# Kernel optimization log

Hardware: AMD Instinct MI355X
Metric: run time of the kernel (lower is better)

The kernel has to match this reference:

```python
import jax, jax.numpy as jnp
import numpy as np

B, T, D, H = 2, 2048, 1024, 16
DH = D // H

def setup_inputs() -> dict:
    key = jax.random.key(0)
    ks = jax.random.split(key, 6)
    s = 0.02
    return {
        "x": jax.random.normal(ks[0], (B, T, D), jnp.float32),
        "Wq": jax.random.normal(ks[1], (D, D), jnp.float32) * s,
        "Wk": jax.random.normal(ks[2], (D, D), jnp.float32) * s,
        "Wv": jax.random.normal(ks[3], (D, D), jnp.float32) * s,
        "Wo": jax.random.normal(ks[4], (D, D), jnp.float32) * s,
        "bo": jnp.zeros((D,), jnp.float32),
    }

def reference(x, Wq, Wk, Wv, Wo, bo):
    Bx, Tx, _ = x.shape
    # project and split heads: [B, H, T, DH]
    q = (x @ Wq).reshape(Bx, Tx, H, DH).transpose(0, 2, 1, 3)
    k = (x @ Wk).reshape(Bx, Tx, H, DH).transpose(0, 2, 1, 3)
    v = (x @ Wv).reshape(Bx, Tx, H, DH).transpose(0, 2, 1, 3)
    scores = jnp.einsum("bhqd,bhkd->bhqk", q, k)  # [B,H,T,T]
    causal = jnp.triu(jnp.ones((Tx, Tx), bool), k=1)  # True above diagonal
    scores = jnp.where(causal, -jnp.inf, scores)
    # original scales AFTER masking (equivalent math)
    w = jax.nn.softmax(scores / jnp.sqrt(jnp.float32(DH)), axis=-1)
    # dropout p=0.0 -> identity
    ctx = jnp.einsum("bhqk,bhkd->bhqd", w, v)
    ctx = ctx.transpose(0, 2, 1, 3).reshape(Bx, Tx, D)
    return ctx @ Wo + bo
```

## Files before the change

kernel.cpp:

```cpp
#include <hip/hip_runtime.h>
#include <hip/hip_bf16.h>


typedef __bf16 bf16x8 __attribute__((ext_vector_type(8)));
typedef __bf16 bf16x4 __attribute__((ext_vector_type(4)));
typedef float  f32x4  __attribute__((ext_vector_type(4)));

#define Bx 2
#define Tx 2048
#define Dx 1024
#define Hx 16
#define DHx 64

__device__ __constant__ unsigned char JTAB[47][3] = {
    {16, 0, 17},
    {31, 0, 16}, {31, 16, 16}, {30, 0, 16}, {15, 0, 16},
    {30, 16, 15}, {29, 0, 15}, {29, 15, 15}, {28, 0, 15}, {14, 0, 15},
    {28, 15, 14}, {27, 0, 14}, {27, 14, 14}, {26, 0, 14}, {13, 0, 14},
    {26, 14, 13}, {25, 0, 13}, {25, 13, 13}, {24, 0, 13}, {12, 0, 13},
    {24, 13, 12}, {23, 0, 12}, {23, 12, 12}, {22, 0, 12}, {11, 0, 12},
    {22, 12, 11}, {21, 0, 11}, {21, 11, 11}, {20, 0, 11}, {10, 0, 11},
    {20, 11, 10}, {19, 0, 10}, {19, 10, 10}, {18, 0, 10}, {9, 0, 10},
    {18, 10, 9}, {17, 0, 9}, {17, 9, 9}, {8, 0, 9},
    {7, 0, 8}, {6, 0, 7}, {5, 0, 6}, {4, 0, 5}, {3, 0, 4}, {2, 0, 3},
    {1, 0, 2}, {0, 0, 1}
};

__global__ __launch_bounds__(256) void prep(const float* __restrict__ x,
                                            const float* __restrict__ W0,
                                            const float* __restrict__ W1,
                                            const float* __restrict__ W2,
                                            const float* __restrict__ W3,
                                            __bf16* __restrict__ xb,
                                            __bf16* __restrict__ Wt) {
    const int z = blockIdx.z;
    if (z == 0) {
        const int blk = blockIdx.y * 16 + blockIdx.x;
        const float* xp = x + (size_t)blk * 16384;
        __bf16* xo = xb + (size_t)blk * 16384;
#pragma unroll
        for (int i = 0; i < 16; i++) {
            float4 v = *(const float4*)(xp + i * 1024 + threadIdx.x * 4);
            bf16x4 o;
            o[0] = (__bf16)v.x; o[1] = (__bf16)v.y; o[2] = (__bf16)v.z; o[3] = (__bf16)v.w;
            *(bf16x4*)(xo + i * 1024 + threadIdx.x * 4) = o;
        }
        return;
    }
    __shared__ float tile[64][65];
    const float* W = (z == 1) ? W0 : (z == 2) ? W1 : (z == 3) ? W2 : W3;
    __bf16* o = Wt + (size_t)(z - 1) * Dx * Dx;
    int k0 = blockIdx.x * 64, n0 = blockIdx.y * 64;
    int t = threadIdx.x;
    int cc = t & 63, rbase = t >> 6;
#pragma unroll
    for (int i = 0; i < 16; i++) {
        int rr = rbase + i * 4;
        tile[rr][cc] = W[(size_t)(k0 + rr) * Dx + n0 + cc];
    }
    __syncthreads();
#pragma unroll
    for (int i = 0; i < 16; i++) {
        int rr = rbase + i * 4;
        o[(size_t)(n0 + rr) * Dx + k0 + cc] = (__bf16)tile[cc][rr];
    }
}

static __device__ __forceinline__ void gload16(const __bf16* g, __bf16* l) {
    __builtin_amdgcn_global_load_lds((const __attribute__((address_space(1))) void*)g,
                                     (__attribute__((address_space(3))) void*)l, 16, 0, 0);
}

__global__ __launch_bounds__(256, 3) void gemm_qkv(const __bf16* __restrict__ A,
                                                   const __bf16* __restrict__ BT,
                                                   __bf16* __restrict__ Qb,
                                                   __bf16* __restrict__ Kb,
                                                   __bf16* __restrict__ Vt) {
    __shared__ __bf16 As[2][128 * 32];
    __shared__ __bf16 Bs[2][128 * 32];
    const int t = threadIdx.x;
    const int lane = t & 63, wave = t >> 6;
    const int lane15 = lane & 15, quad = lane >> 4;
    const int m0 = blockIdx.x * 128, n0 = blockIdx.y * 128;
    const int wm = wave & 1, wn = wave >> 1;

    const int sr = wave * 16 + (lane >> 2);
    const int sc = (lane & 3) * 8;
    const __bf16* Ag = A + (size_t)(m0 + sr) * Dx + sc;
    const __bf16* Bg = BT + (size_t)(n0 + sr) * Dx + sc;
    __bf16* As00 = &As[0][(wave * 16) * 32];
    __bf16* As01 = &As[0][(64 + wave * 16) * 32];
    __bf16* As10 = &As[1][(wave * 16) * 32];
    __bf16* As11 = &As[1][(64 + wave * 16) * 32];
    __bf16* Bs00 = &Bs[0][(wave * 16) * 32];
    __bf16* Bs01 = &Bs[0][(64 + wave * 16) * 32];
    __bf16* Bs10 = &Bs[1][(wave * 16) * 32];
    __bf16* Bs11 = &Bs[1][(64 + wave * 16) * 32];

    f32x4 acc[4][4];
#pragma unroll
    for (int i = 0; i < 4; i++)
#pragma unroll
        for (int j = 0; j < 4; j++) acc[i][j] = (f32x4){0.f, 0.f, 0.f, 0.f};

    for (int k0 = 0; k0 < Dx; k0 += 64) {
        gload16(Ag, As00);
        gload16(Ag + 64 * Dx, As01);
        gload16(Ag + 32, As10);
        gload16(Ag + 64 * Dx + 32, As11);
        gload16(Bg, Bs00);
        gload16(Bg + 64 * Dx, Bs01);
        gload16(Bg + 32, Bs10);
        gload16(Bg + 64 * Dx + 32, Bs11);
        Ag += 64; Bg += 64;
        __syncthreads();
#pragma unroll
        for (int half = 0; half < 2; half++) {
            bf16x8 af[4], bfr[4];
#pragma unroll
            for (int i = 0; i < 4; i++)
                af[i] = *(const bf16x8*)&As[half][(wm * 64 + i * 16 + lane15) * 32 + quad * 8];
#pragma unroll
            for (int j = 0; j < 4; j++)
                bfr[j] = *(const bf16x8*)&Bs[half][(wn * 64 + j * 16 + lane15) * 32 + quad * 8];
#pragma unroll
            for (int mt = 0; mt < 4; mt++)
#pragma unroll
                for (int nt = 0; nt < 4; nt++)
                    acc[mt][nt] = __builtin_amdgcn_mfma_f32_16x16x32_bf16(af[mt], bfr[nt], acc[mt][nt], 0, 0, 0);
        }
        __syncthreads();
    }

    const int z = n0 >> 10;
    if (z < 2) {
        __bf16* outp = z ? Kb : Qb;
        const float scale = z ? 1.0f : 0.18033688011112042f;
#pragma unroll
        for (int mt = 0; mt < 4; mt++)
#pragma unroll
            for (int nt = 0; nt < 4; nt++) {
                const int cc = (n0 + wn * 64 + nt * 16 + lane15) & 1023;
                const int h = cc >> 6, dh = cc & 63;
#pragma unroll
                for (int r4 = 0; r4 < 4; r4++) {
                    const int row = m0 + wm * 64 + mt * 16 + quad * 4 + r4;
                    const int b = row >> 11, tt = row & 2047;
                    outp[(((size_t)(b * Hx + h) * Tx + tt) << 6) + dh] =
                        (__bf16)(acc[mt][nt][r4] * scale);
                }
            }
    } else {
#pragma unroll
        for (int mt = 0; mt < 4; mt++)
#pragma unroll
            for (int nt = 0; nt < 4; nt++) {
                const int cc = (n0 + wn * 64 + nt * 16 + lane15) & 1023;
                const int h = cc >> 6, dh = cc & 63;
#pragma unroll
                for (int r4 = 0; r4 < 4; r4++) {
                    const int row = m0 + wm * 64 + mt * 16 + quad * 4 + r4;
                    const int b = row >> 11, tt = row & 2047;
                    Vt[((size_t)(b * Hx + h) * DHx + dh) * Tx + tt] = (__bf16)acc[mt][nt][r4];
                }
            }
    }
}

__global__ __launch_bounds__(256, 2) void gemm_out(const __bf16* __restrict__ A,
                                                   const __bf16* __restrict__ BT,
                                                   float* __restrict__ outf,
                                                   const float* __restrict__ bias) {
    __shared__ __bf16 As[2][128 * 32];
    __shared__ __bf16 Bs[2][64 * 32];
    const int t = threadIdx.x;
    const int lane = t & 63, wave = t >> 6;
    const int lane15 = lane & 15, quad = lane >> 4;
    const int m0 = blockIdx.x * 128, n0 = blockIdx.y * 64;
    const int wm = wave & 1, wn = wave >> 1;

    const int sr = wave * 16 + (lane >> 2), sc = (lane & 3) * 8;
    const __bf16* Ag = A + (size_t)(m0 + sr) * Dx + sc;
    const __bf16* Bg = BT + (size_t)(n0 + sr) * Dx + sc;
    __bf16* As00 = &As[0][(wave * 16) * 32];
    __bf16* As01 = &As[0][(64 + wave * 16) * 32];
    __bf16* As10 = &As[1][(wave * 16) * 32];
    __bf16* As11 = &As[1][(64 + wave * 16) * 32];
    __bf16* Bs0  = &Bs[0][(wave * 16) * 32];
    __bf16* Bs1  = &Bs[1][(wave * 16) * 32];

    f32x4 acc[4][2];
#pragma unroll
    for (int i = 0; i < 4; i++)
#pragma unroll
        for (int j = 0; j < 2; j++) acc[i][j] = (f32x4){0.f, 0.f, 0.f, 0.f};

    for (int k0 = 0; k0 < Dx; k0 += 64) {
        gload16(Ag, As00);
        gload16(Ag + 64 * Dx, As01);
        gload16(Ag + 32, As10);
        gload16(Ag + 64 * Dx + 32, As11);
        gload16(Bg, Bs0);
        gload16(Bg + 32, Bs1);
        Ag += 64; Bg += 64;
        __syncthreads();
#pragma unroll
        for (int half = 0; half < 2; half++) {
            bf16x8 af[4], bfr[2];
#pragma unroll
            for (int i = 0; i < 4; i++)
                af[i] = *(const bf16x8*)&As[half][(wm * 64 + i * 16 + lane15) * 32 + quad * 8];
#pragma unroll
            for (int j = 0; j < 2; j++)
                bfr[j] = *(const bf16x8*)&Bs[half][(wn * 32 + j * 16 + lane15) * 32 + quad * 8];
#pragma unroll
            for (int mt = 0; mt < 4; mt++)
#pragma unroll
                for (int nt = 0; nt < 2; nt++)
                    acc[mt][nt] = __builtin_amdgcn_mfma_f32_16x16x32_bf16(af[mt], bfr[nt], acc[mt][nt], 0, 0, 0);
        }
        __syncthreads();
    }

#pragma unroll
    for (int mt = 0; mt < 4; mt++)
#pragma unroll
        for (int nt = 0; nt < 2; nt++) {
            const int col = n0 + wn * 32 + nt * 16 + lane15;
#pragma unroll
            for (int r4 = 0; r4 < 4; r4++) {
                const int row = m0 + wm * 64 + mt * 16 + quad * 4 + r4;
                outf[(size_t)row * Dx + col] = acc[mt][nt][r4] + bias[col];
            }
        }
}

__global__ __launch_bounds__(256) void attn_mfma(const __bf16* __restrict__ Q,
                                                 const __bf16* __restrict__ K,
                                                 const __bf16* __restrict__ Vt,
                                                 __bf16* __restrict__ ctx,
                                                 float* __restrict__ o0w,
                                                 float* __restrict__ o1w,
                                                 float* __restrict__ lw) {
    __shared__ __bf16 Ks[64 * 72];
    __shared__ __bf16 Vs[64 * 72];
    __shared__ __bf16 Ps[64 * 72];
    const int t = threadIdx.x;
    const int lane = t & 63, wave = t >> 6;
    const int lane15 = lane & 15, quad = lane >> 4;
    const int id = blockIdx.x;
    const int j = id >> 5, bh = id & 31;
    const int c = JTAB[j][0];
    const int t0 = JTAB[j][1];
    const int ktend = t0 + JTAB[j][2];
    const bool single = (t0 == 0) && (ktend == c + 1);
    const int b = bh >> 4, h = bh & 15;
    const int q0 = c * 64;
    const int qg = q0 + wave * 16 + quad * 4;
    const size_t headoff = ((size_t)(b * Hx + h)) * Tx * DHx;
    const __bf16* Kbase = K + headoff;
    const __bf16* Vbase = Vt + headoff;
    const int sr = t >> 2, sc = (t & 3) * 16;

    bf16x8 qf0, qf1;
    {
        const __bf16* Qp = Q + headoff + (size_t)(q0 + wave * 16 + lane15) * 64 + quad * 8;
        qf0 = *(const bf16x8*)Qp;
        qf1 = *(const bf16x8*)(Qp + 32);
    }
    f32x4 o[4];
#pragma unroll
    for (int i = 0; i < 4; i++) o[i] = (f32x4){0.f, 0.f, 0.f, 0.f};
    float lpart[4] = {0.f, 0.f, 0.f, 0.f};

    bf16x8 kpre0, kpre1, vpre0, vpre1;
    {
        const __bf16* Kp = Kbase + (size_t)(t0 * 64 + sr) * 64 + sc;
        kpre0 = *(const bf16x8*)Kp; kpre1 = *(const bf16x8*)(Kp + 8);
        const __bf16* Vp = Vbase + (size_t)sr * Tx + t0 * 64 + sc;
        vpre0 = *(const bf16x8*)Vp; vpre1 = *(const bf16x8*)(Vp + 8);
    }

    for (int kt = t0; kt < ktend; kt++) {
        __syncthreads();
        *(bf16x8*)&Ks[sr * 72 + sc] = kpre0;
        *(bf16x8*)&Ks[sr * 72 + sc + 8] = kpre1;
        *(bf16x8*)&Vs[sr * 72 + sc] = vpre0;
        *(bf16x8*)&Vs[sr * 72 + sc + 8] = vpre1;
        if (kt + 1 < ktend) {
            const __bf16* Kp = Kbase + (size_t)((kt + 1) * 64 + sr) * 64 + sc;
            kpre0 = *(const bf16x8*)Kp; kpre1 = *(const bf16x8*)(Kp + 8);
            const __bf16* Vp = Vbase + (size_t)sr * Tx + (kt + 1) * 64 + sc;
            vpre0 = *(const bf16x8*)Vp; vpre1 = *(const bf16x8*)(Vp + 8);
        }
        __syncthreads();

        f32x4 s[4];
        __builtin_amdgcn_s_setprio(1);
#pragma unroll
        for (int nt = 0; nt < 4; nt++) {
            s[nt] = (f32x4){0.f, 0.f, 0.f, 0.f};
            bf16x8 b0 = *(const bf16x8*)&Ks[(nt * 16 + lane15) * 72 + quad * 8];
            s[nt] = __builtin_amdgcn_mfma_f32_16x16x32_bf16(qf0, b0, s[nt], 0, 0, 0);
            bf16x8 b1 = *(const bf16x8*)&Ks[(nt * 16 + lane15) * 72 + 32 + quad * 8];
            s[nt] = __builtin_amdgcn_mfma_f32_16x16x32_bf16(qf1, b1, s[nt], 0, 0, 0);
        }
        __builtin_amdgcn_s_setprio(0);

        if (kt == c) {
            const int kbase = kt * 64;
#pragma unroll
            for (int nt = 0; nt < 4; nt++)
#pragma unroll
                for (int reg = 0; reg < 4; reg++) {
                    float e = __builtin_amdgcn_exp2f(s[nt][reg]);
                    if (kbase + nt * 16 + lane15 > qg + reg) e = 0.f;
                    lpart[reg] += e;
                    Ps[(wave * 16 + quad * 4 + reg) * 72 + nt * 16 + lane15] = (__bf16)e;
                }
        } else {
#pragma unroll
            for (int nt = 0; nt < 4; nt++)
#pragma unroll
                for (int reg = 0; reg < 4; reg++) {
                    float e = __builtin_amdgcn_exp2f(s[nt][reg]);
                    lpart[reg] += e;
                    Ps[(wave * 16 + quad * 4 + reg) * 72 + nt * 16 + lane15] = (__bf16)e;
                }
        }

        bf16x8 pa0 = *(const bf16x8*)&Ps[(wave * 16 + lane15) * 72 + quad * 8];
        bf16x8 pa1 = *(const bf16x8*)&Ps[(wave * 16 + lane15) * 72 + 32 + quad * 8];
        __builtin_amdgcn_s_setprio(1);
#pragma unroll
        for (int dt = 0; dt < 4; dt++) {
            bf16x8 vb0 = *(const bf16x8*)&Vs[(dt * 16 + lane15) * 72 + quad * 8];
            o[dt] = __builtin_amdgcn_mfma_f32_16x16x32_bf16(pa0, vb0, o[dt], 0, 0, 0);
            bf16x8 vb1 = *(const bf16x8*)&Vs[(dt * 16 + lane15) * 72 + 32 + quad * 8];
            o[dt] = __builtin_amdgcn_mfma_f32_16x16x32_bf16(pa1, vb1, o[dt], 0, 0, 0);
        }
        __builtin_amdgcn_s_setprio(0);
    }

    float lsum[4];
#pragma unroll
    for (int reg = 0; reg < 4; reg++) {
        float l = lpart[reg];
#pragma unroll
        for (int off = 1; off < 16; off <<= 1) l += __shfl_xor(l, off);
        lsum[reg] = l;
    }

    if (single) {
#pragma unroll
        for (int dt = 0; dt < 4; dt++)
#pragma unroll
            for (int reg = 0; reg < 4; reg++) {
                int q = q0 + wave * 16 + quad * 4 + reg;
                ctx[(((size_t)(b * Tx + q)) * Hx + h) * 64 + dt * 16 + lane15] =
                    (__bf16)(o[dt][reg] / lsum[reg]);
            }
    } else {
        float* op = (t0 == 0) ? o0w : o1w;
        const int tr0 = q0 - 1088 + wave * 16 + quad * 4;
#pragma unroll
        for (int dt = 0; dt < 4; dt++)
#pragma unroll
            for (int reg = 0; reg < 4; reg++)
                op[((size_t)(b * 960 + tr0 + reg) << 10) + h * 64 + dt * 16 + lane15] =
                    o[dt][reg];
        if (lane15 == 0) {
            const int slot = (t0 == 0) ? 0 : 1;
            float* lp = lw + ((size_t)(slot * Bx + b) * Hx + h) * 960 + tr0;
#pragma unroll
            for (int reg = 0; reg < 4; reg++) lp[reg] = lsum[reg];
        }
    }
}

__global__ __launch_bounds__(256) void norm(const float* __restrict__ o0w,
                                            const float* __restrict__ o1w,
                                            const float* __restrict__ lw,
                                            __bf16* __restrict__ ctx) {
    const int r = blockIdx.x;
    const int b = r / 960, tr = r % 960;
    const int tid = threadIdx.x;
    const int h = tid >> 4;
    const size_t rowoff = ((size_t)(b * 960 + tr) << 10) + tid * 4;
    float4 a = *(const float4*)(o0w + rowoff);
    float4 c4 = *(const float4*)(o1w + rowoff);
    const float l0 = lw[((size_t)(0 * Bx + b) * Hx + h) * 960 + tr];
    const float l1 = lw[((size_t)(1 * Bx + b) * Hx + h) * 960 + tr];
    const float inv = 1.f / (l0 + l1);
    bf16x4 o;
    o[0] = (__bf16)((a.x + c4.x) * inv);
    o[1] = (__bf16)((a.y + c4.y) * inv);
    o[2] = (__bf16)((a.z + c4.z) * inv);
    o[3] = (__bf16)((a.w + c4.w) * inv);
    *(bf16x4*)(ctx + (((size_t)(b * Tx + 1088 + tr)) << 10) + tid * 4) = o;
}

extern "C" void kernel_launch(void* const* d_in, const int* in_sizes, int n_in,
                              void* d_out, int out_size, void* d_ws, size_t ws_size,
                              hipStream_t stream) {
    const float* x  = (const float*)d_in[0];
    const float* Wq = (const float*)d_in[1];
    const float* Wk = (const float*)d_in[2];
    const float* Wv = (const float*)d_in[3];
    const float* Wo = (const float*)d_in[4];
    const float* bo = (const float*)d_in[5];
    float* out = (float*)d_out;

    char* ws = (char*)d_ws;
    __bf16* xb  = (__bf16*)(ws + 0);
    __bf16* Wt  = (__bf16*)(ws + (8ull << 20));
    __bf16* Qb  = (__bf16*)(ws + (16ull << 20));
    __bf16* Kb  = (__bf16*)(ws + (24ull << 20));
    __bf16* Vtg = (__bf16*)(ws + (32ull << 20));
    __bf16* ctx = (__bf16*)(ws + (40ull << 20));
    float*  o0w = (float*)(ws + (48ull << 20));
    float*  o1w = (float*)(ws + (56ull << 20));
    float*  lw  = (float*)(ws + (64ull << 20));

    prep<<<dim3(16, 16, 5), 256, 0, stream>>>(x, Wq, Wk, Wv, Wo, xb, Wt);

    gemm_qkv<<<dim3(Bx * Tx / 128, 3 * Dx / 128), 256, 0, stream>>>(xb, Wt, Qb, Kb, Vtg);

    attn_mfma<<<dim3(1504), 256, 0, stream>>>(Qb, Kb, Vtg, ctx, o0w, o1w, lw);

    norm<<<dim3(1920), 256, 0, stream>>>(o0w, o1w, lw, ctx);

    gemm_out<<<dim3(Bx * Tx / 128, Dx / 64), 256, 0, stream>>>(ctx, Wt + 3 * (1u << 20), out, bo);
}
```

Measured before the change: 173.2 us.

## Fuse split-KV combine into attention via atomic last-block-finishes merge

Removes the separate norm kernel that merged two partial attention outputs. Each split block now writes its partial result, fences, and increments a per-tile counter; the second block to arrive reads the other partial and writes the normalized context directly. Counters are zeroed in the prep kernel. This saves a kernel launch and one pass over the partial buffers, at the cost of atomics, fences and a serialized tail on the last-arriving block.

```diff
diff --git a/kernel.cpp b/kernel.cpp
--- a/kernel.cpp
+++ b/kernel.cpp
@@ -32,9 +32,15 @@
                                             const float* __restrict__ W2,
                                             const float* __restrict__ W3,
                                             __bf16* __restrict__ xb,
-                                            __bf16* __restrict__ Wt) {
+                                            __bf16* __restrict__ Wt,
+                                            int* __restrict__ flags) {
     const int z = blockIdx.z;
     if (z == 0) {
+        if (blockIdx.x == 0 && blockIdx.y == 0) {
+            const int tt = threadIdx.x;
+            flags[tt] = 0;
+            if (tt < 480 - 256) flags[256 + tt] = 0;
+        }
         const int blk = blockIdx.y * 16 + blockIdx.x;
         const float* xp = x + (size_t)blk * 16384;
         __bf16* xo = xb + (size_t)blk * 16384;
@@ -241,10 +247,12 @@
                                                  __bf16* __restrict__ ctx,
                                                  float* __restrict__ o0w,
                                                  float* __restrict__ o1w,
-                                                 float* __restrict__ lw) {
+                                                 float* __restrict__ lw,
+                                                 int* __restrict__ flags) {
     __shared__ __bf16 Ks[64 * 72];
     __shared__ __bf16 Vs[64 * 72];
     __shared__ __bf16 Ps[64 * 72];
+    __shared__ int oldflag;
     const int t = threadIdx.x;
     const int lane = t & 63, wave = t >> 6;
     const int lane15 = lane & 15, quad = lane >> 4;
@@ -375,29 +383,30 @@
 #pragma unroll
             for (int reg = 0; reg < 4; reg++) lp[reg] = lsum[reg];
         }
-    }
-}
-
-__global__ __launch_bounds__(256) void norm(const float* __restrict__ o0w,
-                                            const float* __restrict__ o1w,
-                                            const float* __restrict__ lw,
-                                            __bf16* __restrict__ ctx) {
-    const int r = blockIdx.x;
-    const int b = r / 960, tr = r % 960;
-    const int tid = threadIdx.x;
-    const int h = tid >> 4;
-    const size_t rowoff = ((size_t)(b * 960 + tr) << 10) + tid * 4;
-    float4 a = *(const float4*)(o0w + rowoff);
-    float4 c4 = *(const float4*)(o1w + rowoff);
-    const float l0 = lw[((size_t)(0 * Bx + b) * Hx + h) * 960 + tr];
-    const float l1 = lw[((size_t)(1 * Bx + b) * Hx + h) * 960 + tr];
-    const float inv = 1.f / (l0 + l1);
-    bf16x4 o;
-    o[0] = (__bf16)((a.x + c4.x) * inv);
-    o[1] = (__bf16)((a.y + c4.y) * inv);
-    o[2] = (__bf16)((a.z + c4.z) * inv);
-    o[3] = (__bf16)((a.w + c4.w) * inv);
-    *(bf16x4*)(ctx + (((size_t)(b * Tx + 1088 + tr)) << 10) + tid * 4) = o;
+        __threadfence();
+        __syncthreads();
+        if (t == 0) oldflag = atomicAdd(&flags[(b * Hx + h) * 15 + (c - 17)], 1);
+        __syncthreads();
+        if (oldflag == 1) {
+            __threadfence();
+            const float* oo = (t0 == 0) ? o1w : o0w;
+            const int oslot = (t0 == 0) ? 1 : 0;
+            const float* lo = lw + ((size_t)(oslot * Bx + b) * Hx + h) * 960 + tr0;
+            float lother[4];
+#pragma unroll
+            for (int reg = 0; reg < 4; reg++) lother[reg] = lo[reg];
+#pragma unroll
+            for (int dt = 0; dt < 4; dt++)
+#pragma unroll
+                for (int reg = 0; reg < 4; reg++) {
+                    const float other =
+                        oo[((size_t)(b * 960 + tr0 + reg) << 10) + h * 64 + dt * 16 + lane15];
+                    const int q = q0 + wave * 16 + quad * 4 + reg;
+                    ctx[(((size_t)(b * Tx + q)) * Hx + h) * 64 + dt * 16 + lane15] =
+                        (__bf16)((o[dt][reg] + other) / (lsum[reg] + lother[reg]));
+                }
+        }
+    }
 }
 
 extern "C" void kernel_launch(void* const* d_in, const int* in_sizes, int n_in,
@@ -421,14 +430,13 @@
     float*  o0w = (float*)(ws + (48ull << 20));
     float*  o1w = (float*)(ws + (56ull << 20));
     float*  lw  = (float*)(ws + (64ull << 20));
-
-    prep<<<dim3(16, 16, 5), 256, 0, stream>>>(x, Wq, Wk, Wv, Wo, xb, Wt);
+    int*    flg = (int*)(ws + (64ull << 20) + (256u << 10));
+
+    prep<<<dim3(16, 16, 5), 256, 0, stream>>>(x, Wq, Wk, Wv, Wo, xb, Wt, flg);
 
     gemm_qkv<<<dim3(Bx * Tx / 128, 3 * Dx / 128), 256, 0, stream>>>(xb, Wt, Qb, Kb, Vtg);
 
-    attn_mfma<<<dim3(1504), 256, 0, stream>>>(Qb, Kb, Vtg, ctx, o0w, o1w, lw);
-
-    norm<<<dim3(1920), 256, 0, stream>>>(o0w, o1w, lw, ctx);
+    attn_mfma<<<dim3(1504), 256, 0, stream>>>(Qb, Kb, Vtg, ctx, o0w, o1w, lw, flg);
 
     gemm_out<<<dim3(Bx * Tx / 128, Dx / 64), 256, 0, stream>>>(ctx, Wt + 3 * (1u << 20), out, bo);
 }
```

New measurement: 341.7 us. +97.3%, slower.

## Stage V-transpose through LDS for coalesced stores and XOR-swizzle attention LDS

Applied to the files above, without the earlier changes.

In the QKV GEMM, the V output is now transposed through a shared-memory buffer, so each thread writes contiguous 16-byte chunks along T instead of scattered 2-byte stores with stride Tx. In the attention kernel, the padded 72-wide K/V/P tiles are replaced by unpadded 64-wide tiles addressed with an XOR swizzle, which removes LDS bank conflicts and shrinks LDS use. The V path adds extra LDS traffic and barriers to the GEMM epilogue. The extra shared buffer may also reduce occupancy of the GEMM, which is declared with three blocks per CU.

```diff
diff --git a/kernel.cpp b/kernel.cpp
--- a/kernel.cpp
+++ b/kernel.cpp
@@ -71,6 +71,10 @@
                                      (__attribute__((address_space(3))) void*)l, 16, 0, 0);
 }
 
+static __device__ __forceinline__ char* swzp(char* base, int row, int colByte) {
+    return base + row * 128 + (colByte ^ ((row & 7) << 4));
+}
+
 __global__ __launch_bounds__(256, 3) void gemm_qkv(const __bf16* __restrict__ A,
                                                    const __bf16* __restrict__ BT,
                                                    __bf16* __restrict__ Qb,
@@ -78,6 +82,7 @@
                                                    __bf16* __restrict__ Vt) {
     __shared__ __bf16 As[2][128 * 32];
     __shared__ __bf16 Bs[2][128 * 32];
+    __shared__ __bf16 Vbuf[64 * 136];
     const int t = threadIdx.x;
     const int lane = t & 63, wave = t >> 6;
     const int lane15 = lane & 15, quad = lane >> 4;
@@ -151,19 +156,33 @@
                 }
             }
     } else {
-#pragma unroll
-        for (int mt = 0; mt < 4; mt++)
-#pragma unroll
-            for (int nt = 0; nt < 4; nt++) {
-                const int cc = (n0 + wn * 64 + nt * 16 + lane15) & 1023;
-                const int h = cc >> 6, dh = cc & 63;
-#pragma unroll
-                for (int r4 = 0; r4 < 4; r4++) {
-                    const int row = m0 + wm * 64 + mt * 16 + quad * 4 + r4;
-                    const int b = row >> 11, tt = row & 2047;
-                    Vt[((size_t)(b * Hx + h) * DHx + dh) * Tx + tt] = (__bf16)acc[mt][nt][r4];
-                }
+        const int bq = m0 >> 11;
+        const int tt0 = m0 & 2047;
+#pragma unroll
+        for (int p = 0; p < 2; p++) {
+            if (p) __syncthreads();
+            if (wn == p) {
+#pragma unroll
+                for (int mt = 0; mt < 4; mt++)
+#pragma unroll
+                    for (int nt = 0; nt < 4; nt++) {
+                        bf16x4 v4;
+#pragma unroll
+                        for (int r4 = 0; r4 < 4; r4++) v4[r4] = (__bf16)acc[mt][nt][r4];
+                        *(bf16x4*)&Vbuf[(nt * 16 + lane15) * 136 + wm * 64 + mt * 16 + quad * 4] = v4;
+                    }
             }
+            __syncthreads();
+            const int row = t >> 2;
+            const int part = (t & 3) * 32;
+            const int cf = (n0 + p * 64 + row) & 1023;
+            const int h = cf >> 6, dh = cf & 63;
+            __bf16* dst = Vt + ((size_t)(bq * Hx + h) * DHx + dh) * Tx + tt0 + part;
+            const __bf16* srcl = &Vbuf[row * 136 + part];
+#pragma unroll
+            for (int i = 0; i < 4; i++)
+                *(bf16x8*)(dst + i * 8) = *(const bf16x8*)(srcl + i * 8);
+        }
     }
 }
 
@@ -242,9 +261,9 @@
                                                  float* __restrict__ o0w,
                                                  float* __restrict__ o1w,
                                                  float* __restrict__ lw) {
-    __shared__ __bf16 Ks[64 * 72];
-    __shared__ __bf16 Vs[64 * 72];
-    __shared__ __bf16 Ps[64 * 72];
+    __shared__ __bf16 Ks[64 * 64];
+    __shared__ __bf16 Vs[64 * 64];
+    __shared__ __bf16 Ps[64 * 64];
     const int t = threadIdx.x;
     const int lane = t & 63, wave = t >> 6;
     const int lane15 = lane & 15, quad = lane >> 4;
@@ -260,7 +279,12 @@
     const size_t headoff = ((size_t)(b * Hx + h)) * Tx * DHx;
     const __bf16* Kbase = K + headoff;
     const __bf16* Vbase = Vt + headoff;
-    const int sr = t >> 2, sc = (t & 3) * 16;
+    const int sr = t >> 2;
+    const int sce = (t & 3) * 16;
+    const int scB = sce * 2;
+    char* KsB = (char*)Ks;
+    char* VsB = (char*)Vs;
+    char* PsB = (char*)Ps;
 
     bf16x8 qf0, qf1;
     {
@@ -275,22 +299,22 @@
 
     bf16x8 kpre0, kpre1, vpre0, vpre1;
     {
-        const __bf16* Kp = Kbase + (size_t)(t0 * 64 + sr) * 64 + sc;
+        const __bf16* Kp = Kbase + (size_t)(t0 * 64 + sr) * 64 + sce;
         kpre0 = *(const bf16x8*)Kp; kpre1 = *(const bf16x8*)(Kp + 8);
-        const __bf16* Vp = Vbase + (size_t)sr * Tx + t0 * 64 + sc;
+        const __bf16* Vp = Vbase + (size_t)sr * Tx + t0 * 64 + sce;
         vpre0 = *(const bf16x8*)Vp; vpre1 = *(const bf16x8*)(Vp + 8);
     }
 
     for (int kt = t0; kt < ktend; kt++) {
         __syncthreads();
-        *(bf16x8*)&Ks[sr * 72 + sc] = kpre0;
-        *(bf16x8*)&Ks[sr * 72 + sc + 8] = kpre1;
-        *(bf16x8*)&Vs[sr * 72 + sc] = vpre0;
-        *(bf16x8*)&Vs[sr * 72 + sc + 8] = vpre1;
+        *(bf16x8*)swzp(KsB, sr, scB)      = kpre0;
+        *(bf16x8*)swzp(KsB, sr, scB + 16) = kpre1;
+        *(bf16x8*)swzp(VsB, sr, scB)      = vpre0;
+        *(bf16x8*)swzp(VsB, sr, scB + 16) = vpre1;
         if (kt + 1 < ktend) {
-            const __bf16* Kp = Kbase + (size_t)((kt + 1) * 64 + sr) * 64 + sc;
+            const __bf16* Kp = Kbase + (size_t)((kt + 1) * 64 + sr) * 64 + sce;
             kpre0 = *(const bf16x8*)Kp; kpre1 = *(const bf16x8*)(Kp + 8);
-            const __bf16* Vp = Vbase + (size_t)sr * Tx + (kt + 1) * 64 + sc;
+            const __bf16* Vp = Vbase + (size_t)sr * Tx + (kt + 1) * 64 + sce;
             vpre0 = *(const bf16x8*)Vp; vpre1 = *(const bf16x8*)(Vp + 8);
         }
         __syncthreads();
@@ -300,9 +324,9 @@
 #pragma unroll
         for (int nt = 0; nt < 4; nt++) {
             s[nt] = (f32x4){0.f, 0.f, 0.f, 0.f};
-            bf16x8 b0 = *(const bf16x8*)&Ks[(nt * 16 + lane15) * 72 + quad * 8];
+            bf16x8 b0 = *(const bf16x8*)swzp(KsB, nt * 16 + lane15, quad * 16);
             s[nt] = __builtin_amdgcn_mfma_f32_16x16x32_bf16(qf0, b0, s[nt], 0, 0, 0);
-            bf16x8 b1 = *(const bf16x8*)&Ks[(nt * 16 + lane15) * 72 + 32 + quad * 8];
+            bf16x8 b1 = *(const bf16x8*)swzp(KsB, nt * 16 + lane15, 64 + quad * 16);
             s[nt] = __builtin_amdgcn_mfma_f32_16x16x32_bf16(qf1, b1, s[nt], 0, 0, 0);
         }
         __builtin_amdgcn_s_setprio(0);
@@ -316,7 +340,8 @@
                     float e = __builtin_amdgcn_exp2f(s[nt][reg]);
                     if (kbase + nt * 16 + lane15 > qg + reg) e = 0.f;
                     lpart[reg] += e;
-                    Ps[(wave * 16 + quad * 4 + reg) * 72 + nt * 16 + lane15] = (__bf16)e;
+                    *(__bf16*)swzp(PsB, wave * 16 + quad * 4 + reg,
+                                   (nt * 16 + lane15) * 2) = (__bf16)e;
                 }
         } else {
 #pragma unroll
@@ -325,18 +350,19 @@
                 for (int reg = 0; reg < 4; reg++) {
                     float e = __builtin_amdgcn_exp2f(s[nt][reg]);
                     lpart[reg] += e;
-                    Ps[(wave * 16 + quad * 4 + reg) * 72 + nt * 16 + lane15] = (__bf16)e;
+                    *(__bf16*)swzp(PsB, wave * 16 + quad * 4 + reg,
+                                   (nt * 16 + lane15) * 2) = (__bf16)e;
                 }
         }
 
-        bf16x8 pa0 = *(const bf16x8*)&Ps[(wave * 16 + lane15) * 72 + quad * 8];
-        bf16x8 pa1 = *(const bf16x8*)&Ps[(wave * 16 + lane15) * 72 + 32 + quad * 8];
+        bf16x8 pa0 = *(const bf16x8*)swzp(PsB, wave * 16 + lane15, quad * 16);
+        bf16x8 pa1 = *(const bf16x8*)swzp(PsB, wave * 16 + lane15, 64 + quad * 16);
         __builtin_amdgcn_s_setprio(1);
 #pragma unroll
         for (int dt = 0; dt < 4; dt++) {
-            bf16x8 vb0 = *(const bf16x8*)&Vs[(dt * 16 + lane15) * 72 + quad * 8];
+            bf16x8 vb0 = *(const bf16x8*)swzp(VsB, dt * 16 + lane15, quad * 16);
             o[dt] = __builtin_amdgcn_mfma_f32_16x16x32_bf16(pa0, vb0, o[dt], 0, 0, 0);
-            bf16x8 vb1 = *(const bf16x8*)&Vs[(dt * 16 + lane15) * 72 + 32 + quad * 8];
+            bf16x8 vb1 = *(const bf16x8*)swzp(VsB, dt * 16 + lane15, 64 + quad * 16);
             o[dt] = __builtin_amdgcn_mfma_f32_16x16x32_bf16(pa1, vb1, o[dt], 0, 0, 0);
         }
         __builtin_amdgcn_s_setprio(0);
```

New measurement: 170.1 us, median of 3. About the same (-1.8%).
